# Performance work log

Measured on AMD Instinct MI355X. Metric: run time of the kernel, lower is better.

Reference implementation:

```python
import jax, jax.numpy as jnp
import numpy as np

N_CELLS = 10   # nr_cells
CELL = 20      # cell_size (w)
R = 1          # read heads
HID = 128      # controller hidden
IN = 10        # dnc input_size
OUT = 10       # output_dim
CLIP = 20.0
IFACE = R * CELL + 3 * CELL + 5 * R + 3  # 88


def _lstm_step(x, h, c, Wih, Whh, b):
    gates = x @ Wih.T + h @ Whh.T + b
    i, f, g, o = jnp.split(gates, 4, axis=-1)
    c = jax.nn.sigmoid(f) * c + jax.nn.sigmoid(i) * jnp.tanh(g)
    h = jax.nn.sigmoid(o) * jnp.tanh(c)
    return h, c


def _content(mem, keys, strengths):
    # mem (b,n,w), keys (b,k,w), strengths (b,k) -> (b,k,n)
    dot = jnp.einsum('bkw,bnw->bkn', keys, mem)
    kn = jnp.linalg.norm(keys, axis=-1, keepdims=True)
    mn = jnp.linalg.norm(mem, axis=-1)[:, None, :]
    return jax.nn.softmax(dot / (kn * mn + 1e-6) * strengths[..., None], axis=-1)


def _allocate(usage):
    u = 1e-6 + (1.0 - 1e-6) * usage
    idx = jnp.argsort(u, axis=-1)                      # ascending usage
    su = jnp.take_along_axis(u, idx, axis=-1)
    excl = jnp.concatenate([jnp.ones_like(su[:, :1]), jnp.cumprod(su, axis=-1)[:, :-1]], axis=-1)
    sa = (1.0 - su) * excl                             # sorted allocation weights
    inv = jnp.argsort(idx, axis=-1)
    return jnp.take_along_axis(sa, inv, axis=-1)


def _dnc_forward(x, W_ih0, W_hh0, b0, W_ih1, W_hh1, b1, W_if, b_if, W_out, b_out):
    B, T, _ = x.shape
    dt = x.dtype
    z = lambda *s: jnp.zeros(s, dt)
    carry0 = (z(B, HID), z(B, HID), z(B, HID), z(B, HID),   # h0,c0,h1,c1
              z(B, N_CELLS, CELL),                          # memory
              z(B, N_CELLS),                                # usage
              z(B, N_CELLS),                                # precedence
              z(B, N_CELLS, N_CELLS),                       # link matrix
              z(B, R, N_CELLS),                             # read weights
              z(B, N_CELLS),                                # write weights
              z(B, R, CELL))                                # read vectors
    eye = jnp.eye(N_CELLS, dtype=dt)

    def step(carry, xt):
        h0, c0, h1, c1, mem, usage, prec, link, rw, ww, rv = carry
        inp = jnp.concatenate([xt, rv.reshape(B, R * CELL)], axis=-1)
        h0, c0 = _lstm_step(inp, h0, c0, W_ih0, W_hh0, b0)
        h1, c1 = _lstm_step(h0, h1, c1, W_ih1, W_hh1, b1)
        ctrl = jnp.clip(h1, -CLIP, CLIP)
        xi = ctrl @ W_if.T + b_if                            # (B, 88)
        rk = jnp.tanh(xi[:, 0:20]).reshape(B, R, CELL)       # read keys
        rs = jax.nn.softplus(xi[:, 20:21])                   # read strengths
        wk = jnp.tanh(xi[:, 21:41]).reshape(B, 1, CELL)      # write key
        ws = jax.nn.softplus(xi[:, 41:42])                   # write strength
        er = jax.nn.sigmoid(xi[:, 42:62])                    # erase vector
        wv = jnp.tanh(xi[:, 62:82])                          # write vector
        fg = jax.nn.sigmoid(xi[:, 82:83])                    # free gates
        ga = jax.nn.sigmoid(xi[:, 83:84])                    # allocation gate
        gw = jax.nn.sigmoid(xi[:, 84:85])                    # write gate
        modes = jax.nn.softmax(xi[:, 85:88].reshape(B, R, 3), axis=-1)
        # --- write ---
        psi = jnp.prod(1.0 - fg[:, :, None] * rw, axis=1)    # retention (b,n)
        usage = (usage + ww - usage * ww) * psi
        alloc = _allocate(usage)
        cw = _content(mem, wk, ws)[:, 0]                     # (b,n)
        ww = gw * (ga * alloc + (1.0 - ga) * cw)
        mem = mem * (1.0 - ww[:, :, None] * er[:, None, :]) + ww[:, :, None] * wv[:, None, :]
        link = (1.0 - ww[:, :, None] - ww[:, None, :]) * link + ww[:, :, None] * prec[:, None, :]
        link = link * (1.0 - eye)
        prec = (1.0 - ww.sum(-1, keepdims=True)) * prec + ww
        # --- read ---
        fwd_w = jnp.einsum('brn,bmn->brm', rw, link)         # L @ w  (forward)
        bwd_w = jnp.einsum('brn,bnm->brm', rw, link)         # L^T @ w (backward)
        cr = _content(mem, rk, rs)
        rw = modes[..., 0:1] * bwd_w + modes[..., 1:2] * cr + modes[..., 2:3] * fwd_w
        rv = jnp.einsum('brn,bnw->brw', rw, mem)
        o = jnp.concatenate([ctrl, rv.reshape(B, R * CELL)], axis=-1)
        y = o @ W_out.T + b_out
        return (h0, c0, h1, c1, mem, usage, prec, link, rw, ww, rv), y

    _, ys = jax.lax.scan(step, carry0, jnp.swapaxes(x, 0, 1))
    return ys[-1]  # output[:, -1, :]


def setup_inputs() -> dict:
    key = jax.random.key(0)
    ks = jax.random.split(key, 8)
    s = 0.08
    B, T = 512, 512
    return {
        'x': jax.random.normal(ks[0], (B, T, IN), jnp.float32),
        'W_ih0': s * jax.random.normal(ks[1], (4 * HID, IN + R * CELL), jnp.float32),
        'W_hh0': s * jax.random.normal(ks[2], (4 * HID, HID), jnp.float32),
        'b0': jnp.zeros((4 * HID,), jnp.float32),
        'W_ih1': s * jax.random.normal(ks[3], (4 * HID, HID), jnp.float32),
        'W_hh1': s * jax.random.normal(ks[4], (4 * HID, HID), jnp.float32),
        'b1': jnp.zeros((4 * HID,), jnp.float32),
        'W_if': s * jax.random.normal(ks[5], (IFACE, HID), jnp.float32),
        'b_if': jnp.zeros((IFACE,), jnp.float32),
        'W_out': s * jax.random.normal(ks[6], (OUT, HID + R * CELL), jnp.float32),
        'b_out': jnp.zeros((OUT,), jnp.float32),
    }


def reference(x, W_ih0, W_hh0, b0, W_ih1, W_hh1, b1, W_if, b_if, W_out, b_out):
    return _dnc_forward(x, W_ih0, W_hh0, b0, W_ih1, W_hh1, b1, W_if, b_if, W_out, b_out)
```

## Files before the change

kernel.cpp:

```cpp
#include <hip/hip_runtime.h>
#include <math.h>

#define NT 512
#define NB 512
#define HID 128
#define NIN 10
#define NC 10
#define CW 20
#define NIF 88
#define NOUT 10
#define GB 2
#define BLK 512

typedef _Float16 h1;
typedef _Float16 h2 __attribute__((ext_vector_type(2)));

__device__ __forceinline__ float sigf(float x) { return 1.0f / (1.0f + expf(-x)); }
__device__ __forceinline__ float splus(float x) { return fmaxf(x, 0.0f) + log1pf(expf(-fabsf(x))); }

__device__ __forceinline__ float dot2(h2 a, h2 b, float c) {
#if __has_builtin(__builtin_amdgcn_fdot2)
  return __builtin_amdgcn_fdot2(a, b, c, false);
#else
  c += (float)a.x * (float)b.x;
  c += (float)a.y * (float)b.y;
  return c;
#endif
}

#define LDSFENCE() do { asm volatile("s_waitcnt lgkmcnt(0)" ::: "memory"); \
                        __builtin_amdgcn_sched_barrier(0); } while (0)

#define BC(f) __builtin_bit_cast(h2, f)

#define DOTF4(W, fa, fb)                                   \
  a0 = dot2(BC((W).x), BC((fa).x), a0);                    \
  a1 = dot2(BC((W).x), BC((fb).x), a1);                    \
  a2 = dot2(BC((W).y), BC((fa).y), a2);                    \
  a3 = dot2(BC((W).y), BC((fb).y), a3);                    \
  a0 = dot2(BC((W).z), BC((fa).z), a0);                    \
  a1 = dot2(BC((W).z), BC((fb).z), a1);                    \
  a2 = dot2(BC((W).w), BC((fa).w), a2);                    \
  a3 = dot2(BC((W).w), BC((fb).w), a3);

#define LSTEP(W, i, Pa, Pb) { float4 fa = (Pa)[i], fb = (Pb)[i]; DOTF4(W, fa, fb) }

__device__ __forceinline__ float4 pack8(const float* p) {
  h2 v0, v1, v2, v3;
  v0.x=(h1)p[0]; v0.y=(h1)p[1]; v1.x=(h1)p[2]; v1.y=(h1)p[3];
  v2.x=(h1)p[4]; v2.y=(h1)p[5]; v3.x=(h1)p[6]; v3.y=(h1)p[7];
  float4 r;
  r.x=__builtin_bit_cast(float,v0); r.y=__builtin_bit_cast(float,v1);
  r.z=__builtin_bit_cast(float,v2); r.w=__builtin_bit_cast(float,v3);
  return r;
}
__device__ __forceinline__ float4 pack6z(const float* p) {
  h2 v0, v1, v2, v3;
  v0.x=(h1)p[0]; v0.y=(h1)p[1]; v1.x=(h1)p[2]; v1.y=(h1)p[3];
  v2.x=(h1)p[4]; v2.y=(h1)p[5]; v3.x=(h1)0.f;  v3.y=(h1)0.f;
  float4 r;
  r.x=__builtin_bit_cast(float,v0); r.y=__builtin_bit_cast(float,v1);
  r.z=__builtin_bit_cast(float,v2); r.w=__builtin_bit_cast(float,v3);
  return r;
}

__global__ __launch_bounds__(256) void dnc_pack_kernel(
    const float* __restrict__ Wih1, const float* __restrict__ Whh1, float4* __restrict__ ws)
{
  int i = blockIdx.x * 256 + threadIdx.x;
  if (i < 16*512) {
    int c = i >> 9, rr = i & 511;
    ws[i] = pack8(Whh1 + (size_t)rr*HID + 8*c);
  } else if (i < 18*512) {
    int j = i - 16*512; int c2 = j >> 9, rr = j & 511;
    ws[i] = pack8(Wih1 + (size_t)rr*HID + (14 + c2)*8);
  }
}

__global__ __launch_bounds__(BLK)
void dnc_stream_kernel(
    const float* __restrict__ x,
    const float* __restrict__ Wih0, const float* __restrict__ Whh0, const float* __restrict__ b0,
    const float* __restrict__ Wih1, const float* __restrict__ Whh1, const float* __restrict__ b1,
    const float* __restrict__ Wif,  const float* __restrict__ bif,
    const float* __restrict__ Wout, const float* __restrict__ bout,
    const float4* __restrict__ wsT,
    float* __restrict__ out)
{
  __shared__ __align__(16) float4 s_wih1T[14][512];
  __shared__ __align__(16) float4 s_wifT[16*89];
  __shared__ __align__(16) float s_g[GB][512];
  __shared__ __align__(16) float s_fp[NIF][9];
  __shared__ float s_bif[NIF];
  __shared__ __align__(16) h1   s_inph[GB][32];
  __shared__ __align__(16) h1   s_h0h[GB][HID];
  __shared__ __align__(16) h1   s_h1h[GB][HID];
  __shared__ __align__(16) h1   s_ctrlh[GB][HID];
  __shared__ __align__(16) float s_ctrl[GB][HID];
  __shared__ __align__(16) float s_mem[GB][NC][CW];
  __shared__ float s_rk[GB][CW], s_wk[GB][CW], s_er[GB][CW], s_wv[GB][CW];
  __shared__ float s_mraw[GB][3];
  __shared__ float s_sc[GB][8];
  __shared__ float s_usage[GB][NC], s_u[GB][NC];
  __shared__ float s_prec[GB][NC], s_prec2[GB][NC];
  __shared__ float s_link[GB][NC][NC];
  __shared__ float s_rw[GB][NC], s_ww[GB][NC];
  __shared__ float s_rv[GB][CW];
  __shared__ float s_cw[GB][NC], s_cr[GB][NC], s_fwd[GB][NC], s_bwd[GB][NC];

  const int tid = threadIdx.x;
  const int bg  = blockIdx.x * GB;
  const int r   = tid;

  float4 A0,A1,A2,A3;
  float4 B0,B1,B2,B3,B4,B5,B6,B7,B8,B9,B10,B11,B12,B13,B14,B15;
  float b0r, b1r;
  {
    const float* p = Wih0 + (size_t)r * (NIN + CW);
    A0=pack8(p); A1=pack8(p+8); A2=pack8(p+16); A3=pack6z(p+24);
    const float* q0 = Whh0 + (size_t)r*HID;
    B0 =pack8(q0);    B1 =pack8(q0+8);  B2 =pack8(q0+16);  B3 =pack8(q0+24);
    B4 =pack8(q0+32); B5 =pack8(q0+40); B6 =pack8(q0+48);  B7 =pack8(q0+56);
    B8 =pack8(q0+64); B9 =pack8(q0+72); B10=pack8(q0+80);  B11=pack8(q0+88);
    B12=pack8(q0+96); B13=pack8(q0+104);B14=pack8(q0+112); B15=pack8(q0+120);
    b0r = b0[r]; b1r = b1[r];
  }

  for (int idx = tid; idx < 14*512; idx += BLK) {
    int c = idx >> 9, rr = idx & 511;
    s_wih1T[c][rr] = pack8(Wih1 + (size_t)rr*HID + 8*c);
  }
  for (int idx = tid; idx < 16*NIF; idx += BLK) {
    int j = idx / NIF, q = idx - j*NIF;
    s_wifT[j*89 + q] = pack8(Wif + (size_t)q*HID + 8*j);
  }
  if (tid < NIF) s_bif[tid] = bif[tid];

  if (tid < GB*HID) { int b=tid>>7, j=tid&127;
    s_h0h[b][j]=(h1)0.f; s_h1h[b][j]=(h1)0.f; s_ctrlh[b][j]=(h1)0.f; s_ctrl[b][j]=0.f; }
  for (int i = tid; i < GB*NC*CW; i += BLK) { int b=i/(NC*CW), e=i%(NC*CW);
    s_mem[b][e/CW][e%CW]=0.f; }
  for (int i = tid; i < GB*NC*NC; i += BLK) { int b=i/(NC*NC), e=i%(NC*NC);
    s_link[b][e/NC][e%NC]=0.f; }
  if (tid < GB*NC) { int b=tid/NC, n=tid%NC;
    s_usage[b][n]=0.f; s_prec[b][n]=0.f; s_rw[b][n]=0.f; s_ww[b][n]=0.f; }
  if (tid < GB*CW) { int b=tid/CW, c=tid%CW; s_rv[b][c]=0.f; }
  if (tid < GB*32) { int b=tid>>5, i=tid&31;
    float v = 0.f;
    if (i < NIN) v = x[((size_t)(bg+b)*NT + 0)*NIN + i];
    s_inph[b][i] = (h1)v;
  }
  float c0r = 0.f, c1r = 0.f;
  __syncthreads();

  for (int t = 0; t < NT; ++t) {
    {
      float a0=b0r, a1=b0r, a2=0.f, a3=0.f;
      const float4* Ia = (const float4*)s_inph[0];
      const float4* Ib = (const float4*)s_inph[1];
      LSTEP(A0,0,Ia,Ib) LSTEP(A1,1,Ia,Ib) LSTEP(A2,2,Ia,Ib) LSTEP(A3,3,Ia,Ib)
      const float4* Ha = (const float4*)s_h0h[0];
      const float4* Hb = (const float4*)s_h0h[1];
      LSTEP(B0,0,Ha,Hb)   LSTEP(B1,1,Ha,Hb)   LSTEP(B2,2,Ha,Hb)   LSTEP(B3,3,Ha,Hb)
      LSTEP(B4,4,Ha,Hb)   LSTEP(B5,5,Ha,Hb)   LSTEP(B6,6,Ha,Hb)   LSTEP(B7,7,Ha,Hb)
      LSTEP(B8,8,Ha,Hb)   LSTEP(B9,9,Ha,Hb)   LSTEP(B10,10,Ha,Hb) LSTEP(B11,11,Ha,Hb)
      LSTEP(B12,12,Ha,Hb) LSTEP(B13,13,Ha,Hb) LSTEP(B14,14,Ha,Hb) LSTEP(B15,15,Ha,Hb)
      s_g[0][r] = a0+a2; s_g[1][r] = a1+a3;
    }
    __syncthreads();

    if (tid < GB*HID) {
      int b = tid>>7, j = tid&127;
      float gi=s_g[b][j], gf=s_g[b][HID+j], gg=s_g[b][2*HID+j], go=s_g[b][3*HID+j];
      float c = sigf(gf)*c0r + sigf(gi)*tanhf(gg);
      c0r = c;
      float h = sigf(go)*tanhf(c);
      s_h0h[b][j] = (h1)h;
    }
    __syncthreads();

    {
      unsigned lnd = 0;
      asm volatile("" : "+v"(lnd));
      const float4* WS = (const float4*)((const char*)wsT + lnd);
      float a0=b1r, a1=b1r, a2=0.f, a3=0.f;
      const float4* Ha = (const float4*)s_h0h[0];
      const float4* Hb = (const float4*)s_h0h[1];
      const float4* Ga = (const float4*)s_h1h[0];
      const float4* Gb = (const float4*)s_h1h[1];
      float4 t0 = WS[16*512 + tid];
      float4 t1 = WS[17*512 + tid];
      float4 u0 = WS[0*512 + tid];
      float4 u1 = WS[1*512 + tid];
      { float4 w=s_wih1T[ 0][r]; LSTEP(w, 0,Ha,Hb) }
      { float4 w=s_wih1T[ 1][r]; LSTEP(w, 1,Ha,Hb) }
      { float4 w=s_wih1T[ 2][r]; LSTEP(w, 2,Ha,Hb) }
      { float4 w=s_wih1T[ 3][r]; LSTEP(w, 3,Ha,Hb) }
      { float4 w=s_wih1T[ 4][r]; LSTEP(w, 4,Ha,Hb) }
      { float4 w=s_wih1T[ 5][r]; LSTEP(w, 5,Ha,Hb) }
      { float4 w=s_wih1T[ 6][r]; LSTEP(w, 6,Ha,Hb) }
      { float4 w=s_wih1T[ 7][r]; LSTEP(w, 7,Ha,Hb) }
      { float4 w=s_wih1T[ 8][r]; LSTEP(w, 8,Ha,Hb) }
      { float4 w=s_wih1T[ 9][r]; LSTEP(w, 9,Ha,Hb) }
      { float4 w=s_wih1T[10][r]; LSTEP(w,10,Ha,Hb) }
      { float4 w=s_wih1T[11][r]; LSTEP(w,11,Ha,Hb) }
      { float4 w=s_wih1T[12][r]; LSTEP(w,12,Ha,Hb) }
      { float4 w=s_wih1T[13][r]; LSTEP(w,13,Ha,Hb) }
      LSTEP(t0,14,Ha,Hb) LSTEP(t1,15,Ha,Hb)
      t0 = WS[ 2*512+tid]; t1 = WS[ 3*512+tid];
      LSTEP(u0, 0,Ga,Gb) LSTEP(u1, 1,Ga,Gb)
      u0 = WS[ 4*512+tid]; u1 = WS[ 5*512+tid];
      LSTEP(t0, 2,Ga,Gb) LSTEP(t1, 3,Ga,Gb)
      t0 = WS[ 6*512+tid]; t1 = WS[ 7*512+tid];
      LSTEP(u0, 4,Ga,Gb) LSTEP(u1, 5,Ga,Gb)
      u0 = WS[ 8*512+tid]; u1 = WS[ 9*512+tid];
      LSTEP(t0, 6,Ga,Gb) LSTEP(t1, 7,Ga,Gb)
      t0 = WS[10*512+tid]; t1 = WS[11*512+tid];
      LSTEP(u0, 8,Ga,Gb) LSTEP(u1, 9,Ga,Gb)
      u0 = WS[12*512+tid]; u1 = WS[13*512+tid];
      LSTEP(t0,10,Ga,Gb) LSTEP(t1,11,Ga,Gb)
      t0 = WS[14*512+tid]; t1 = WS[15*512+tid];
      LSTEP(u0,12,Ga,Gb) LSTEP(u1,13,Ga,Gb)
      LSTEP(t0,14,Ga,Gb) LSTEP(t1,15,Ga,Gb)
      s_g[0][r] = a0+a2; s_g[1][r] = a1+a3;
    }
    __syncthreads();

    if (tid < GB*HID) {
      int b = tid>>7, j = tid&127;
      float gi=s_g[b][j], gf=s_g[b][HID+j], gg=s_g[b][2*HID+j], go=s_g[b][3*HID+j];
      float c = sigf(gf)*c1r + sigf(gi)*tanhf(gg);
      c1r = c;
      float h = sigf(go)*tanhf(c);
      float ctl = fminf(fmaxf(h, -20.f), 20.f);
      s_h1h[b][j] = (h1)h;
      s_ctrl[b][j] = ctl;
      s_ctrlh[b][j] = (h1)ctl;
    }
    __syncthreads();

    if (tid < 4*NIF) {
      int q = tid >> 2, c = tid & 3;
      float a0=0.f, a1=0.f, a2=0.f, a3=0.f;
      const float4* Ca = (const float4*)s_ctrlh[0];
      const float4* Cb = (const float4*)s_ctrlh[1];
      float4 w0 = s_wifT[(4*c+0)*89 + q];
      float4 w1 = s_wifT[(4*c+1)*89 + q];
      float4 w2 = s_wifT[(4*c+2)*89 + q];
      float4 w3 = s_wifT[(4*c+3)*89 + q];
      LSTEP(w0, 4*c+0, Ca, Cb) LSTEP(w1, 4*c+1, Ca, Cb)
      LSTEP(w2, 4*c+2, Ca, Cb) LSTEP(w3, 4*c+3, Ca, Cb)
      s_fp[q][2*c  ] = a0+a2;
      s_fp[q][2*c+1] = a1+a3;
    }
    __syncthreads();

    if (tid < 64) {
      const int lane = tid;
      float xv = 0.f;
      if (lane >= GB*CW && lane < GB*CW + GB*NIN && (t+1) < NT) {
        int q = lane - GB*CW, b = q/NIN, i = q%NIN;
        xv = x[((size_t)(bg+b)*NT + (t+1))*NIN + i];
      }

      #pragma unroll
      for (int e = lane; e < 2*NIF; e += 64) {
        int b = e & 1, q = e >> 1;
        float a = s_bif[q];
        #pragma unroll
        for (int c = 0; c < 4; ++c) a += s_fp[q][2*c+b];
        if      (q < 20)  s_rk[b][q]    = tanhf(a);
        else if (q == 20) s_sc[b][0]    = splus(a);
        else if (q < 41)  s_wk[b][q-21] = tanhf(a);
        else if (q == 41) s_sc[b][1]    = splus(a);
        else if (q < 62)  s_er[b][q-42] = sigf(a);
        else if (q < 82)  s_wv[b][q-62] = tanhf(a);
        else if (q == 82) s_sc[b][2]    = sigf(a);
        else if (q == 83) s_sc[b][3]    = sigf(a);
        else if (q == 84) s_sc[b][4]    = sigf(a);
        else              s_mraw[b][q-85] = a;
      }
      LDSFENCE();

      if (lane < GB*NC) {
        int b = lane/NC, n = lane%NC;
        float fg = s_sc[b][2];
        float psi = 1.f - fg * s_rw[b][n];
        float u = s_usage[b][n], w = s_ww[b][n];
        u = (u + w - u*w) * psi;
        s_usage[b][n] = u;
        s_u[b][n] = 1e-6f + (1.0f - 1e-6f) * u;
        float dot=0.f, mn=0.f, kn=0.f;
        #pragma unroll
        for (int c = 0; c < CW; ++c) {
          float m = s_mem[b][n][c], k = s_wk[b][c];
          dot += k*m; mn += m*m; kn += k*k;
        }
        s_cw[b][n] = dot / (sqrtf(kn)*sqrtf(mn) + 1e-6f) * s_sc[b][1];
      } else if (lane < GB*NC + GB) {
        int b = lane - GB*NC;
        float m0=s_mraw[b][0], m1=s_mraw[b][1], m2=s_mraw[b][2];
        float mm = fmaxf(m0, fmaxf(m1, m2));
        float e0=expf(m0-mm), e1=expf(m1-mm), e2=expf(m2-mm);
        float es = e0+e1+e2;
        s_sc[b][5]=e0/es; s_sc[b][6]=e1/es; s_sc[b][7]=e2/es;
      }
      LDSFENCE();

      if (lane < GB*NC) {
        int b = lane/NC, n = lane%NC;
        float mx = -1e30f;
        #pragma unroll
        for (int m = 0; m < NC; ++m) mx = fmaxf(mx, s_cw[b][m]);
        float sm = 0.f;
        #pragma unroll
        for (int m = 0; m < NC; ++m) sm += expf(s_cw[b][m]-mx);
        float cwv = expf(s_cw[b][n]-mx) / sm;
        float un = s_u[b][n];
        float excl = 1.f;
        #pragma unroll
        for (int m = 0; m < NC; ++m) {
          float um = s_u[b][m];
          bool before = (um < un) || (um == un && m < n);
          excl *= before ? um : 1.f;
        }
        float alloc = (1.f - un) * excl;
        float ga = s_sc[b][3], gw = s_sc[b][4];
        s_ww[b][n] = gw * (ga*alloc + (1.f-ga)*cwv);
      }
      LDSFENCE();

      #pragma unroll
      for (int e = lane; e < GB*NC*CW; e += 64) {
        int b = e/(NC*CW), rr = (e%(NC*CW))/CW, c = e%CW;
        float w = s_ww[b][rr];
        s_mem[b][rr][c] = s_mem[b][rr][c] * (1.f - w*s_er[b][c]) + w*s_wv[b][c];
      }
      #pragma unroll
      for (int e = lane; e < GB*NC*NC; e += 64) {
        int b = e/(NC*NC), i = (e%(NC*NC))/NC, j = e%NC;
        float wi = s_ww[b][i], wj = s_ww[b][j];
        float l = (1.f - wi - wj)*s_link[b][i][j] + wi*s_prec[b][j];
        s_link[b][i][j] = (i==j) ? 0.f : l;
      }
      if (lane < GB*NC) {
        int b = lane/NC, n = lane%NC;
        float sw2 = 0.f;
        #pragma unroll
        for (int m = 0; m < NC; ++m) sw2 += s_ww[b][m];
        s_prec2[b][n] = (1.f - sw2)*s_prec[b][n] + s_ww[b][n];
      }
      LDSFENCE();

      if (lane < GB*NC) {
        int b = lane/NC, m = lane%NC;
        s_prec[b][m] = s_prec2[b][m];
        float a = 0.f;
        #pragma unroll
        for (int n = 0; n < NC; ++n) a += s_rw[b][n]*s_link[b][m][n];
        s_fwd[b][m] = a;
      } else if (lane < 2*GB*NC) {
        int q = lane - GB*NC, b = q/NC, m = q%NC;
        float a = 0.f;
        #pragma unroll
        for (int n = 0; n < NC; ++n) a += s_rw[b][n]*s_link[b][n][m];
        s_bwd[b][m] = a;
      } else if (lane < 3*GB*NC) {
        int q = lane - 2*GB*NC, b = q/NC, n = q%NC;
        float dot=0.f, mn=0.f, kn=0.f;
        #pragma unroll
        for (int c = 0; c < CW; ++c) {
          float m = s_mem[b][n][c], k = s_rk[b][c];
          dot += k*m; mn += m*m; kn += k*k;
        }
        s_cr[b][n] = dot/(sqrtf(kn)*sqrtf(mn)+1e-6f) * s_sc[b][0];
      }
      LDSFENCE();

      if (lane < GB*NC) {
        int b = lane/NC, n = lane%NC;
        float mx = -1e30f;
        #pragma unroll
        for (int m = 0; m < NC; ++m) mx = fmaxf(mx, s_cr[b][m]);
        float sm = 0.f;
        #pragma unroll
        for (int m = 0; m < NC; ++m) sm += expf(s_cr[b][m]-mx);
        float cr = expf(s_cr[b][n]-mx)/sm;
        s_rw[b][n] = s_sc[b][5]*s_bwd[b][n] + s_sc[b][6]*cr + s_sc[b][7]*s_fwd[b][n];
      }
      LDSFENCE();

      if (lane < GB*CW) {
        int b = lane/CW, c = lane%CW;
        float a = 0.f;
        #pragma unroll
        for (int n = 0; n < NC; ++n) a += s_rw[b][n]*s_mem[b][n][c];
        s_rv[b][c] = a;
        s_inph[b][NIN + c] = (h1)a;
      } else if (lane < GB*CW + GB*NIN && (t+1) < NT) {
        int q = lane - GB*CW, b = q/NIN, i = q%NIN;
        s_inph[b][i] = (h1)xv;
      }
    }
    __syncthreads();
  }

  if (tid < GB*NOUT) {
    int b = tid/NOUT, o = tid%NOUT;
    float a = bout[o];
    const float* Wr = Wout + o*(HID+CW);
    #pragma unroll 4
    for (int k = 0; k < HID; ++k) a += Wr[k]*s_ctrl[b][k];
    #pragma unroll
    for (int c = 0; c < CW; ++c) a += Wr[HID+c]*s_rv[b][c];
    out[(size_t)(bg+b)*NOUT + o] = a;
  }
}

extern "C" void kernel_launch(void* const* d_in, const int* in_sizes, int n_in,
                              void* d_out, int out_size, void* d_ws, size_t ws_size,
                              hipStream_t stream) {
  (void)in_sizes; (void)n_in; (void)out_size; (void)ws_size;
  const float* x    = (const float*)d_in[0];
  const float* Wih0 = (const float*)d_in[1];
  const float* Whh0 = (const float*)d_in[2];
  const float* b0   = (const float*)d_in[3];
  const float* Wih1 = (const float*)d_in[4];
  const float* Whh1 = (const float*)d_in[5];
  const float* b1   = (const float*)d_in[6];
  const float* Wif  = (const float*)d_in[7];
  const float* bif  = (const float*)d_in[8];
  const float* Wout = (const float*)d_in[9];
  const float* bout = (const float*)d_in[10];
  float* out = (float*)d_out;
  float4* ws = (float4*)d_ws;

  dnc_pack_kernel<<<dim3(36), dim3(256), 0, stream>>>(Wih1, Whh1, ws);
  dnc_stream_kernel<<<dim3(NB/GB), dim3(BLK), 0, stream>>>(
      x, Wih0, Whh0, b0, Wih1, Whh1, b1, Wif, bif, Wout, bout, ws, out);
}
```

Measured before the change: 6.005 ms.

## Overlap DNC memory tail with next step's h-dependent LSTM matvecs

Moves the serial DNC memory/read tail (run by one wave) to the start of the next timestep, so it runs at the same time as the layer-0 Whh·h0 and layer-1 Whh·h1 matvecs, which do not depend on the read vector. The read-vector part of layer-0's input projection is split out and applied after a barrier, and x is double-buffered. One end-of-step barrier is removed. It also swaps the math functions for fast __expf/rcp approximations, which costs some accuracy, and the 64 threads running the tail now also carry the matvec work.

```diff
diff --git a/kernel.cpp b/kernel.cpp
--- a/kernel.cpp
+++ b/kernel.cpp
@@ -15,8 +15,14 @@
 typedef _Float16 h1;
 typedef _Float16 h2 __attribute__((ext_vector_type(2)));
 
-__device__ __forceinline__ float sigf(float x) { return 1.0f / (1.0f + expf(-x)); }
-__device__ __forceinline__ float splus(float x) { return fmaxf(x, 0.0f) + log1pf(expf(-fabsf(x))); }
+__device__ __forceinline__ float rcpf(float x) { return __builtin_amdgcn_rcpf(x); }
+__device__ __forceinline__ float sigf(float x) { return rcpf(1.0f + __expf(-x)); }
+__device__ __forceinline__ float tanhf_(float x) {
+  float xc = fminf(fmaxf(x, -15.f), 15.f);
+  float e = __expf(2.f * xc);
+  return (e - 1.f) * rcpf(e + 1.f);
+}
+__device__ __forceinline__ float splus(float x) { return fmaxf(x, 0.0f) + __logf(1.f + __expf(-fabsf(x))); }
 
 __device__ __forceinline__ float dot2(h2 a, h2 b, float c) {
 #if __has_builtin(__builtin_amdgcn_fdot2)
@@ -49,15 +55,6 @@
   h2 v0, v1, v2, v3;
   v0.x=(h1)p[0]; v0.y=(h1)p[1]; v1.x=(h1)p[2]; v1.y=(h1)p[3];
   v2.x=(h1)p[4]; v2.y=(h1)p[5]; v3.x=(h1)p[6]; v3.y=(h1)p[7];
-  float4 r;
-  r.x=__builtin_bit_cast(float,v0); r.y=__builtin_bit_cast(float,v1);
-  r.z=__builtin_bit_cast(float,v2); r.w=__builtin_bit_cast(float,v3);
-  return r;
-}
-__device__ __forceinline__ float4 pack6z(const float* p) {
-  h2 v0, v1, v2, v3;
-  v0.x=(h1)p[0]; v0.y=(h1)p[1]; v1.x=(h1)p[2]; v1.y=(h1)p[3];
-  v2.x=(h1)p[4]; v2.y=(h1)p[5]; v3.x=(h1)0.f;  v3.y=(h1)0.f;
   float4 r;
   r.x=__builtin_bit_cast(float,v0); r.y=__builtin_bit_cast(float,v1);
   r.z=__builtin_bit_cast(float,v2); r.w=__builtin_bit_cast(float,v3);
@@ -78,7 +75,7 @@
 }
 
 __global__ __launch_bounds__(BLK)
-void dnc_stream_kernel(
+void dnc_olap_kernel(
     const float* __restrict__ x,
     const float* __restrict__ Wih0, const float* __restrict__ Whh0, const float* __restrict__ b0,
     const float* __restrict__ Wih1, const float* __restrict__ Whh1, const float* __restrict__ b1,
@@ -92,7 +89,8 @@
   __shared__ __align__(16) float s_g[GB][512];
   __shared__ __align__(16) float s_fp[NIF][9];
   __shared__ float s_bif[NIF];
-  __shared__ __align__(16) h1   s_inph[GB][32];
+  __shared__ __align__(16) h1   s_xbuf[2][GB][16];
+  __shared__ __align__(16) h1   s_rvh[GB][24];
   __shared__ __align__(16) h1   s_h0h[GB][HID];
   __shared__ __align__(16) h1   s_h1h[GB][HID];
   __shared__ __align__(16) h1   s_ctrlh[GB][HID];
@@ -112,12 +110,20 @@
   const int bg  = blockIdx.x * GB;
   const int r   = tid;
 
-  float4 A0,A1,A2,A3;
+  float4 A0,A1,A2,A3,A4;
   float4 B0,B1,B2,B3,B4,B5,B6,B7,B8,B9,B10,B11,B12,B13,B14,B15;
   float b0r, b1r;
   {
     const float* p = Wih0 + (size_t)r * (NIN + CW);
-    A0=pack8(p); A1=pack8(p+8); A2=pack8(p+16); A3=pack6z(p+24);
+    A0 = pack8(p);
+    { h2 v0,z; v0.x=(h1)p[8]; v0.y=(h1)p[9]; z.x=(h1)0.f; z.y=(h1)0.f;
+      float4 f; f.x=__builtin_bit_cast(float,v0); f.y=__builtin_bit_cast(float,z);
+      f.z=f.y; f.w=f.y; A1=f; }
+    A2 = pack8(p+10); A3 = pack8(p+18);
+    { h2 v0,v1,z; v0.x=(h1)p[26]; v0.y=(h1)p[27]; v1.x=(h1)p[28]; v1.y=(h1)p[29];
+      z.x=(h1)0.f; z.y=(h1)0.f;
+      float4 f; f.x=__builtin_bit_cast(float,v0); f.y=__builtin_bit_cast(float,v1);
+      f.z=__builtin_bit_cast(float,z); f.w=f.z; A4=f; }
     const float* q0 = Whh0 + (size_t)r*HID;
     B0 =pack8(q0);    B1 =pack8(q0+8);  B2 =pack8(q0+16);  B3 =pack8(q0+24);
     B4 =pack8(q0+32); B5 =pack8(q0+40); B6 =pack8(q0+48);  B7 =pack8(q0+56);
@@ -145,26 +151,213 @@
   if (tid < GB*NC) { int b=tid/NC, n=tid%NC;
     s_usage[b][n]=0.f; s_prec[b][n]=0.f; s_rw[b][n]=0.f; s_ww[b][n]=0.f; }
   if (tid < GB*CW) { int b=tid/CW, c=tid%CW; s_rv[b][c]=0.f; }
-  if (tid < GB*32) { int b=tid>>5, i=tid&31;
+  if (tid < GB*24) { int b=tid/24, c=tid%24; s_rvh[b][c]=(h1)0.f; }
+  if (tid < 2*GB*16) { int u=tid, d=u>>5, b=(u>>4)&1, i=u&15;
     float v = 0.f;
-    if (i < NIN) v = x[((size_t)(bg+b)*NT + 0)*NIN + i];
-    s_inph[b][i] = (h1)v;
+    if (d == 0 && i < NIN) v = x[((size_t)(bg+b)*NT + 0)*NIN + i];
+    s_xbuf[d][b][i] = (h1)v;
   }
   float c0r = 0.f, c1r = 0.f;
   __syncthreads();
 
+  auto dnc_tail = [&](int lane) {
+    #pragma unroll
+    for (int e = lane; e < 2*NIF; e += 64) {
+      int b = e & 1, q = e >> 1;
+      float a = s_bif[q];
+      #pragma unroll
+      for (int c = 0; c < 4; ++c) a += s_fp[q][2*c+b];
+      if      (q < 20)  s_rk[b][q]    = tanhf_(a);
+      else if (q == 20) s_sc[b][0]    = splus(a);
+      else if (q < 41)  s_wk[b][q-21] = tanhf_(a);
+      else if (q == 41) s_sc[b][1]    = splus(a);
+      else if (q < 62)  s_er[b][q-42] = sigf(a);
+      else if (q < 82)  s_wv[b][q-62] = tanhf_(a);
+      else if (q == 82) s_sc[b][2]    = sigf(a);
+      else if (q == 83) s_sc[b][3]    = sigf(a);
+      else if (q == 84) s_sc[b][4]    = sigf(a);
+      else              s_mraw[b][q-85] = a;
+    }
+    LDSFENCE();
+
+    if (lane < GB*NC) {
+      int b = lane/NC, n = lane%NC;
+      float fg = s_sc[b][2];
+      float psi = 1.f - fg * s_rw[b][n];
+      float u = s_usage[b][n], w = s_ww[b][n];
+      u = (u + w - u*w) * psi;
+      s_usage[b][n] = u;
+      s_u[b][n] = 1e-6f + (1.0f - 1e-6f) * u;
+      float dot=0.f, mn=0.f, kn=0.f;
+      #pragma unroll
+      for (int c = 0; c < CW; ++c) {
+        float m = s_mem[b][n][c], k = s_wk[b][c];
+        dot += k*m; mn += m*m; kn += k*k;
+      }
+      s_cw[b][n] = dot * rcpf(sqrtf(kn)*sqrtf(mn) + 1e-6f) * s_sc[b][1];
+    } else if (lane < GB*NC + GB) {
+      int b = lane - GB*NC;
+      float m0=s_mraw[b][0], m1=s_mraw[b][1], m2=s_mraw[b][2];
+      float mm = fmaxf(m0, fmaxf(m1, m2));
+      float e0=__expf(m0-mm), e1=__expf(m1-mm), e2=__expf(m2-mm);
+      float es = rcpf(e0+e1+e2);
+      s_sc[b][5]=e0*es; s_sc[b][6]=e1*es; s_sc[b][7]=e2*es;
+    }
+    LDSFENCE();
+
+    if (lane < GB*NC) {
+      int b = lane/NC, n = lane%NC;
+      float mx = -1e30f;
+      #pragma unroll
+      for (int m = 0; m < NC; ++m) mx = fmaxf(mx, s_cw[b][m]);
+      float sm = 0.f;
+      #pragma unroll
+      for (int m = 0; m < NC; ++m) sm += __expf(s_cw[b][m]-mx);
+      float cwv = __expf(s_cw[b][n]-mx) * rcpf(sm);
+      float un = s_u[b][n];
+      float excl = 1.f;
+      #pragma unroll
+      for (int m = 0; m < NC; ++m) {
+        float um = s_u[b][m];
+        bool before = (um < un) || (um == un && m < n);
+        excl *= before ? um : 1.f;
+      }
+      float alloc = (1.f - un) * excl;
+      float ga = s_sc[b][3], gw = s_sc[b][4];
+      s_ww[b][n] = gw * (ga*alloc + (1.f-ga)*cwv);
+    }
+    LDSFENCE();
+
+    #pragma unroll
+    for (int e = lane; e < GB*NC*CW; e += 64) {
+      int b = e/(NC*CW), rr = (e%(NC*CW))/CW, c = e%CW;
+      float w = s_ww[b][rr];
+      s_mem[b][rr][c] = s_mem[b][rr][c] * (1.f - w*s_er[b][c]) + w*s_wv[b][c];
+    }
+    #pragma unroll
+    for (int e = lane; e < GB*NC*NC; e += 64) {
+      int b = e/(NC*NC), i = (e%(NC*NC))/NC, j = e%NC;
+      float wi = s_ww[b][i], wj = s_ww[b][j];
+      float l = (1.f - wi - wj)*s_link[b][i][j] + wi*s_prec[b][j];
+      s_link[b][i][j] = (i==j) ? 0.f : l;
+    }
+    if (lane < GB*NC) {
+      int b = lane/NC, n = lane%NC;
+      float sw2 = 0.f;
+      #pragma unroll
+      for (int m = 0; m < NC; ++m) sw2 += s_ww[b][m];
+      s_prec2[b][n] = (1.f - sw2)*s_prec[b][n] + s_ww[b][n];
+    }
+    LDSFENCE();
+
+    if (lane < GB*NC) {
+      int b = lane/NC, m = lane%NC;
+      s_prec[b][m] = s_prec2[b][m];
+      float a = 0.f;
+      #pragma unroll
+      for (int n = 0; n < NC; ++n) a += s_rw[b][n]*s_link[b][m][n];
+      s_fwd[b][m] = a;
+    } else if (lane < 2*GB*NC) {
+      int q = lane - GB*NC, b = q/NC, m = q%NC;
+      float a = 0.f;
+      #pragma unroll
+      for (int n = 0; n < NC; ++n) a += s_rw[b][n]*s_link[b][n][m];
+      s_bwd[b][m] = a;
+    } else if (lane < 3*GB*NC) {
+      int q = lane - 2*GB*NC, b = q/NC, n = q%NC;
+      float dot=0.f, mn=0.f, kn=0.f;
+      #pragma unroll
+      for (int c = 0; c < CW; ++c) {
+        float m = s_mem[b][n][c], k = s_rk[b][c];
+        dot += k*m; mn += m*m; kn += k*k;
+      }
+      s_cr[b][n] = dot * rcpf(sqrtf(kn)*sqrtf(mn)+1e-6f) * s_sc[b][0];
+    }
+    LDSFENCE();
+
+    if (lane < GB*NC) {
+      int b = lane/NC, n = lane%NC;
+      float mx = -1e30f;
+      #pragma unroll
+      for (int m = 0; m < NC; ++m) mx = fmaxf(mx, s_cr[b][m]);
+      float sm = 0.f;
+      #pragma unroll
+      for (int m = 0; m < NC; ++m) sm += __expf(s_cr[b][m]-mx);
+      float cr = __expf(s_cr[b][n]-mx)*rcpf(sm);
+      s_rw[b][n] = s_sc[b][5]*s_bwd[b][n] + s_sc[b][6]*cr + s_sc[b][7]*s_fwd[b][n];
+    }
+    LDSFENCE();
+
+    if (lane < GB*CW) {
+      int b = lane/CW, c = lane%CW;
+      float a = 0.f;
+      #pragma unroll
+      for (int n = 0; n < NC; ++n) a += s_rw[b][n]*s_mem[b][n][c];
+      s_rv[b][c] = a;
+      s_rvh[b][c] = (h1)a;
+    }
+  };
+
   for (int t = 0; t < NT; ++t) {
+    if (tid >= 448) {
+      const int lane = tid - 448;
+      float xv = 0.f;
+      if (lane < GB*NIN && (t+1) < NT) {
+        int b = lane/NIN, i = lane%NIN;
+        xv = x[((size_t)(bg+b)*NT + (t+1))*NIN + i];
+      }
+      if (t > 0) dnc_tail(lane);
+      if (lane < GB*NIN && (t+1) < NT) {
+        int b = lane/NIN, i = lane%NIN;
+        s_xbuf[(t+1)&1][b][i] = (h1)xv;
+      }
+    }
+    unsigned lnd = 0;
+    asm volatile("" : "+v"(lnd));
+    const float4* WS = (const float4*)((const char*)wsT + lnd);
+    float4 u0 = WS[0*512+tid], u1 = WS[1*512+tid];
+    float4 t0 = WS[2*512+tid], t1 = WS[3*512+tid];
+    float r0a, r0b, g1a, g1b;
     {
       float a0=b0r, a1=b0r, a2=0.f, a3=0.f;
-      const float4* Ia = (const float4*)s_inph[0];
-      const float4* Ib = (const float4*)s_inph[1];
-      LSTEP(A0,0,Ia,Ib) LSTEP(A1,1,Ia,Ib) LSTEP(A2,2,Ia,Ib) LSTEP(A3,3,Ia,Ib)
+      const float4* Xa = (const float4*)&s_xbuf[t&1][0][0];
+      const float4* Xb = (const float4*)&s_xbuf[t&1][1][0];
+      LSTEP(A0,0,Xa,Xb) LSTEP(A1,1,Xa,Xb)
       const float4* Ha = (const float4*)s_h0h[0];
       const float4* Hb = (const float4*)s_h0h[1];
       LSTEP(B0,0,Ha,Hb)   LSTEP(B1,1,Ha,Hb)   LSTEP(B2,2,Ha,Hb)   LSTEP(B3,3,Ha,Hb)
       LSTEP(B4,4,Ha,Hb)   LSTEP(B5,5,Ha,Hb)   LSTEP(B6,6,Ha,Hb)   LSTEP(B7,7,Ha,Hb)
       LSTEP(B8,8,Ha,Hb)   LSTEP(B9,9,Ha,Hb)   LSTEP(B10,10,Ha,Hb) LSTEP(B11,11,Ha,Hb)
       LSTEP(B12,12,Ha,Hb) LSTEP(B13,13,Ha,Hb) LSTEP(B14,14,Ha,Hb) LSTEP(B15,15,Ha,Hb)
+      r0a = a0+a2; r0b = a1+a3;
+    }
+    {
+      float a0=0.f, a1=0.f, a2=0.f, a3=0.f;
+      const float4* Ga = (const float4*)s_h1h[0];
+      const float4* Gb = (const float4*)s_h1h[1];
+      LSTEP(u0, 0,Ga,Gb) LSTEP(u1, 1,Ga,Gb)
+      u0 = WS[ 4*512+tid]; u1 = WS[ 5*512+tid];
+      LSTEP(t0, 2,Ga,Gb) LSTEP(t1, 3,Ga,Gb)
+      t0 = WS[ 6*512+tid]; t1 = WS[ 7*512+tid];
+      LSTEP(u0, 4,Ga,Gb) LSTEP(u1, 5,Ga,Gb)
+      u0 = WS[ 8*512+tid]; u1 = WS[ 9*512+tid];
+      LSTEP(t0, 6,Ga,Gb) LSTEP(t1, 7,Ga,Gb)
+      t0 = WS[10*512+tid]; t1 = WS[11*512+tid];
+      LSTEP(u0, 8,Ga,Gb) LSTEP(u1, 9,Ga,Gb)
+      u0 = WS[12*512+tid]; u1 = WS[13*512+tid];
+      LSTEP(t0,10,Ga,Gb) LSTEP(t1,11,Ga,Gb)
+      t0 = WS[14*512+tid]; t1 = WS[15*512+tid];
+      LSTEP(u0,12,Ga,Gb) LSTEP(u1,13,Ga,Gb)
+      LSTEP(t0,14,Ga,Gb) LSTEP(t1,15,Ga,Gb)
+      g1a = a0+a2; g1b = a1+a3;
+    }
+    __syncthreads();
+
+    {
+      float a0=r0a, a1=r0b, a2=0.f, a3=0.f;
+      const float4* Ra = (const float4*)&s_rvh[0][0];
+      const float4* Rb = (const float4*)&s_rvh[1][0];
+      LSTEP(A2,0,Ra,Rb) LSTEP(A3,1,Ra,Rb) LSTEP(A4,2,Ra,Rb)
       s_g[0][r] = a0+a2; s_g[1][r] = a1+a3;
     }
     __syncthreads();
@@ -172,26 +365,18 @@
     if (tid < GB*HID) {
       int b = tid>>7, j = tid&127;
       float gi=s_g[b][j], gf=s_g[b][HID+j], gg=s_g[b][2*HID+j], go=s_g[b][3*HID+j];
-      float c = sigf(gf)*c0r + sigf(gi)*tanhf(gg);
+      float c = sigf(gf)*c0r + sigf(gi)*tanhf_(gg);
       c0r = c;
-      float h = sigf(go)*tanhf(c);
+      float h = sigf(go)*tanhf_(c);
       s_h0h[b][j] = (h1)h;
     }
     __syncthreads();
 
     {
-      unsigned lnd = 0;
-      asm volatile("" : "+v"(lnd));
-      const float4* WS = (const float4*)((const char*)wsT + lnd);
-      float a0=b1r, a1=b1r, a2=0.f, a3=0.f;
+      float4 v0 = WS[16*512+tid], v1 = WS[17*512+tid];
+      float a0 = g1a + b1r, a1 = g1b + b1r, a2=0.f, a3=0.f;
       const float4* Ha = (const float4*)s_h0h[0];
       const float4* Hb = (const float4*)s_h0h[1];
-      const float4* Ga = (const float4*)s_h1h[0];
-      const float4* Gb = (const float4*)s_h1h[1];
-      float4 t0 = WS[16*512 + tid];
-      float4 t1 = WS[17*512 + tid];
-      float4 u0 = WS[0*512 + tid];
-      float4 u1 = WS[1*512 + tid];
       { float4 w=s_wih1T[ 0][r]; LSTEP(w, 0,Ha,Hb) }
       { float4 w=s_wih1T[ 1][r]; LSTEP(w, 1,Ha,Hb) }
       { float4 w=s_wih1T[ 2][r]; LSTEP(w, 2,Ha,Hb) }
@@ -206,22 +391,7 @@
       { float4 w=s_wih1T[11][r]; LSTEP(w,11,Ha,Hb) }
       { float4 w=s_wih1T[12][r]; LSTEP(w,12,Ha,Hb) }
       { float4 w=s_wih1T[13][r]; LSTEP(w,13,Ha,Hb) }
-      LSTEP(t0,14,Ha,Hb) LSTEP(t1,15,Ha,Hb)
-      t0 = WS[ 2*512+tid]; t1 = WS[ 3*512+tid];
-      LSTEP(u0, 0,Ga,Gb) LSTEP(u1, 1,Ga,Gb)
-      u0 = WS[ 4*512+tid]; u1 = WS[ 5*512+tid];
-      LSTEP(t0, 2,Ga,Gb) LSTEP(t1, 3,Ga,Gb)
-      t0 = WS[ 6*512+tid]; t1 = WS[ 7*512+tid];
-      LSTEP(u0, 4,Ga,Gb) LSTEP(u1, 5,Ga,Gb)
-      u0 = WS[ 8*512+tid]; u1 = WS[ 9*512+tid];
-      LSTEP(t0, 6,Ga,Gb) LSTEP(t1, 7,Ga,Gb)
-      t0 = WS[10*512+tid]; t1 = WS[11*512+tid];
-      LSTEP(u0, 8,Ga,Gb) LSTEP(u1, 9,Ga,Gb)
-      u0 = WS[12*512+tid]; u1 = WS[13*512+tid];
-      LSTEP(t0,10,Ga,Gb) LSTEP(t1,11,Ga,Gb)
-      t0 = WS[14*512+tid]; t1 = WS[15*512+tid];
-      LSTEP(u0,12,Ga,Gb) LSTEP(u1,13,Ga,Gb)
-      LSTEP(t0,14,Ga,Gb) LSTEP(t1,15,Ga,Gb)
+      LSTEP(v0,14,Ha,Hb) LSTEP(v1,15,Ha,Hb)
       s_g[0][r] = a0+a2; s_g[1][r] = a1+a3;
     }
     __syncthreads();
@@ -229,9 +399,9 @@
     if (tid < GB*HID) {
       int b = tid>>7, j = tid&127;
       float gi=s_g[b][j], gf=s_g[b][HID+j], gg=s_g[b][2*HID+j], go=s_g[b][3*HID+j];
-      float c = sigf(gf)*c1r + sigf(gi)*tanhf(gg);
+      float c = sigf(gf)*c1r + sigf(gi)*tanhf_(gg);
       c1r = c;
-      float h = sigf(go)*tanhf(c);
+      float h = sigf(go)*tanhf_(c);
       float ctl = fminf(fmaxf(h, -20.f), 20.f);
       s_h1h[b][j] = (h1)h;
       s_ctrl[b][j] = ctl;
@@ -254,156 +424,10 @@
       s_fp[q][2*c+1] = a1+a3;
     }
     __syncthreads();
-
-    if (tid < 64) {
-      const int lane = tid;
-      float xv = 0.f;
-      if (lane >= GB*CW && lane < GB*CW + GB*NIN && (t+1) < NT) {
-        int q = lane - GB*CW, b = q/NIN, i = q%NIN;
-        xv = x[((size_t)(bg+b)*NT + (t+1))*NIN + i];
-      }
-
-      #pragma unroll
-      for (int e = lane; e < 2*NIF; e += 64) {
-        int b = e & 1, q = e >> 1;
-        float a = s_bif[q];
-        #pragma unroll
-        for (int c = 0; c < 4; ++c) a += s_fp[q][2*c+b];
-        if      (q < 20)  s_rk[b][q]    = tanhf(a);
-        else if (q == 20) s_sc[b][0]    = splus(a);
-        else if (q < 41)  s_wk[b][q-21] = tanhf(a);
-        else if (q == 41) s_sc[b][1]    = splus(a);
-        else if (q < 62)  s_er[b][q-42] = sigf(a);
-        else if (q < 82)  s_wv[b][q-62] = tanhf(a);
-        else if (q == 82) s_sc[b][2]    = sigf(a);
-        else if (q == 83) s_sc[b][3]    = sigf(a);
-        else if (q == 84) s_sc[b][4]    = sigf(a);
-        else              s_mraw[b][q-85] = a;
-      }
-      LDSFENCE();
-
-      if (lane < GB*NC) {
-        int b = lane/NC, n = lane%NC;
-        float fg = s_sc[b][2];
-        float psi = 1.f - fg * s_rw[b][n];
-        float u = s_usage[b][n], w = s_ww[b][n];
-        u = (u + w - u*w) * psi;
-        s_usage[b][n] = u;
-        s_u[b][n] = 1e-6f + (1.0f - 1e-6f) * u;
-        float dot=0.f, mn=0.f, kn=0.f;
-        #pragma unroll
-        for (int c = 0; c < CW; ++c) {
-          float m = s_mem[b][n][c], k = s_wk[b][c];
-          dot += k*m; mn += m*m; kn += k*k;
-        }
-        s_cw[b][n] = dot / (sqrtf(kn)*sqrtf(mn) + 1e-6f) * s_sc[b][1];
-      } else if (lane < GB*NC + GB) {
-        int b = lane - GB*NC;
-        float m0=s_mraw[b][0], m1=s_mraw[b][1], m2=s_mraw[b][2];
-        float mm = fmaxf(m0, fmaxf(m1, m2));
-        float e0=expf(m0-mm), e1=expf(m1-mm), e2=expf(m2-mm);
-        float es = e0+e1+e2;
-        s_sc[b][5]=e0/es; s_sc[b][6]=e1/es; s_sc[b][7]=e2/es;
-      }
-      LDSFENCE();
-
-      if (lane < GB*NC) {
-        int b = lane/NC, n = lane%NC;
-        float mx = -1e30f;
-        #pragma unroll
-        for (int m = 0; m < NC; ++m) mx = fmaxf(mx, s_cw[b][m]);
-        float sm = 0.f;
-        #pragma unroll
-        for (int m = 0; m < NC; ++m) sm += expf(s_cw[b][m]-mx);
-        float cwv = expf(s_cw[b][n]-mx) / sm;
-        float un = s_u[b][n];
-        float excl = 1.f;
-        #pragma unroll
-        for (int m = 0; m < NC; ++m) {
-          float um = s_u[b][m];
-          bool before = (um < un) || (um == un && m < n);
-          excl *= before ? um : 1.f;
-        }
-        float alloc = (1.f - un) * excl;
-        float ga = s_sc[b][3], gw = s_sc[b][4];
-        s_ww[b][n] = gw * (ga*alloc + (1.f-ga)*cwv);
-      }
-      LDSFENCE();
-
-      #pragma unroll
-      for (int e = lane; e < GB*NC*CW; e += 64) {
-        int b = e/(NC*CW), rr = (e%(NC*CW))/CW, c = e%CW;
-        float w = s_ww[b][rr];
-        s_mem[b][rr][c] = s_mem[b][rr][c] * (1.f - w*s_er[b][c]) + w*s_wv[b][c];
-      }
-      #pragma unroll
-      for (int e = lane; e < GB*NC*NC; e += 64) {
-        int b = e/(NC*NC), i = (e%(NC*NC))/NC, j = e%NC;
-        float wi = s_ww[b][i], wj = s_ww[b][j];
-        float l = (1.f - wi - wj)*s_link[b][i][j] + wi*s_prec[b][j];
-        s_link[b][i][j] = (i==j) ? 0.f : l;
-      }
-      if (lane < GB*NC) {
-        int b = lane/NC, n = lane%NC;
-        float sw2 = 0.f;
-        #pragma unroll
-        for (int m = 0; m < NC; ++m) sw2 += s_ww[b][m];
-        s_prec2[b][n] = (1.f - sw2)*s_prec[b][n] + s_ww[b][n];
-      }
-      LDSFENCE();
-
-      if (lane < GB*NC) {
-        int b = lane/NC, m = lane%NC;
-        s_prec[b][m] = s_prec2[b][m];
-        float a = 0.f;
-        #pragma unroll
-        for (int n = 0; n < NC; ++n) a += s_rw[b][n]*s_link[b][m][n];
-        s_fwd[b][m] = a;
-      } else if (lane < 2*GB*NC) {
-        int q = lane - GB*NC, b = q/NC, m = q%NC;
-        float a = 0.f;
-        #pragma unroll
-        for (int n = 0; n < NC; ++n) a += s_rw[b][n]*s_link[b][n][m];
-        s_bwd[b][m] = a;
-      } else if (lane < 3*GB*NC) {
-        int q = lane - 2*GB*NC, b = q/NC, n = q%NC;
-        float dot=0.f, mn=0.f, kn=0.f;
-        #pragma unroll
-        for (int c = 0; c < CW; ++c) {
-          float m = s_mem[b][n][c], k = s_rk[b][c];
-          dot += k*m; mn += m*m; kn += k*k;
-        }
-        s_cr[b][n] = dot/(sqrtf(kn)*sqrtf(mn)+1e-6f) * s_sc[b][0];
-      }
-      LDSFENCE();
-
-      if (lane < GB*NC) {
-        int b = lane/NC, n = lane%NC;
-        float mx = -1e30f;
-        #pragma unroll
-        for (int m = 0; m < NC; ++m) mx = fmaxf(mx, s_cr[b][m]);
-        float sm = 0.f;
-        #pragma unroll
-        for (int m = 0; m < NC; ++m) sm += expf(s_cr[b][m]-mx);
-        float cr = expf(s_cr[b][n]-mx)/sm;
-        s_rw[b][n] = s_sc[b][5]*s_bwd[b][n] + s_sc[b][6]*cr + s_sc[b][7]*s_fwd[b][n];
-      }
-      LDSFENCE();
-
-      if (lane < GB*CW) {
-        int b = lane/CW, c = lane%CW;
-        float a = 0.f;
-        #pragma unroll
-        for (int n = 0; n < NC; ++n) a += s_rw[b][n]*s_mem[b][n][c];
-        s_rv[b][c] = a;
-        s_inph[b][NIN + c] = (h1)a;
-      } else if (lane < GB*CW + GB*NIN && (t+1) < NT) {
-        int q = lane - GB*CW, b = q/NIN, i = q%NIN;
-        s_inph[b][i] = (h1)xv;
-      }
-    }
-    __syncthreads();
-  }
+  }
+
+  if (tid >= 448) dnc_tail(tid - 448);
+  __syncthreads();
 
   if (tid < GB*NOUT) {
     int b = tid/NOUT, o = tid%NOUT;
@@ -436,6 +460,6 @@
   float4* ws = (float4*)d_ws;
 
   dnc_pack_kernel<<<dim3(36), dim3(256), 0, stream>>>(Wih1, Whh1, ws);
-  dnc_stream_kernel<<<dim3(NB/GB), dim3(BLK), 0, stream>>>(
+  dnc_olap_kernel<<<dim3(NB/GB), dim3(BLK), 0, stream>>>(
       x, Wih0, Whh0, b0, Wih1, Whh1, b1, Wif, bif, Wout, bout, ws, out);
 }
```

New measurement: 6.119 ms. About the same (+1.9%).
